# Kernel optimization log

Measured on AMD Instinct MI355X. Metric: run time of the kernel, lower is better.

The kernel has to match this reference:

```python
import jax, jax.numpy as jnp
import numpy as np

B, T, D = 8, 16384, 128


def setup_inputs() -> dict:
    key = jax.random.key(0)
    ks = jax.random.split(key, 14)
    sc = lambda fan_in: 1.0 / np.sqrt(fan_in)
    x = jax.random.normal(ks[0], (B, T, D), jnp.float32)
    return {
        "x": x,
        # BindingField (scale 0): bind_key / bind_query Linear(D, D//2)
        "Wk": jax.random.normal(ks[1], (D, D // 2), jnp.float32) * sc(D),
        "bk": jnp.zeros((D // 2,), jnp.float32),
        "Wq": jax.random.normal(ks[2], (D, D // 2), jnp.float32) * sc(D),
        "bq": jnp.zeros((D // 2,), jnp.float32),
        # aggregator (scale 0): Linear(D,D) -> LayerNorm(D) -> ReLU -> Linear(D,D)
        "Wa1": jax.random.normal(ks[3], (D, D), jnp.float32) * sc(D),
        "ba1": jnp.zeros((D,), jnp.float32),
        "ln_g": jnp.ones((D,), jnp.float32),
        "ln_b": jnp.zeros((D,), jnp.float32),
        "Wa2": jax.random.normal(ks[4], (D, D), jnp.float32) * sc(D),
        "ba2": jnp.zeros((D,), jnp.float32),
        # downward_influence (scale 0): Linear(D,D)
        "Wd": jax.random.normal(ks[5], (D, D), jnp.float32) * sc(D),
        "bd": jnp.zeros((D,), jnp.float32),
    }


def reference(x, Wk, bk, Wq, bq, Wa1, ba1, ln_g, ln_b, Wa2, ba2, Wd, bd):
    Bn, Tn, Dn = x.shape
    BIND_THRESHOLD = 0.5
    LN_EPS = 1e-5

    # ---- BindingField: binding strength between adjacent tokens ----
    keys = x[:, :-1] @ Wk + bk                       # [B, T-1, D/2]
    queries = x[:, 1:] @ Wq + bq                     # [B, T-1, D/2]
    strength = jax.nn.sigmoid((keys * queries).sum(-1) / float(np.sqrt(Dn // 2)))
    bind = strength > BIND_THRESHOLD                 # [B, T-1]

    # chunk_starts: token 0 always starts; token t starts iff NOT bound to t-1
    chunk_starts = jnp.concatenate([jnp.ones((Bn, 1), bool), ~bind], axis=1)
    seg = jnp.cumsum(chunk_starts.astype(jnp.int32), axis=1) - 1  # [B, T] chunk id per token

    # ---- aggregate_chunks: ragged mean-pool via segment_sum (pad to T chunk slots) ----
    seg_flat = (seg + jnp.arange(Bn, dtype=jnp.int32)[:, None] * Tn).reshape(-1)
    sums = jax.ops.segment_sum(x.reshape(-1, Dn), seg_flat, num_segments=Bn * Tn)
    counts = jax.ops.segment_sum(jnp.ones((Bn * Tn,), x.dtype), seg_flat,
                                 num_segments=Bn * Tn)
    chunk_mean = (sums / jnp.maximum(counts, 1.0)[:, None]).reshape(Bn, Tn, Dn)

    # aggregator MLP: Linear -> LayerNorm -> ReLU -> Linear
    h = chunk_mean @ Wa1 + ba1
    mu = h.mean(-1, keepdims=True)
    var = ((h - mu) ** 2).mean(-1, keepdims=True)    # biased var, as torch LayerNorm
    h = (h - mu) * jax.lax.rsqrt(var + LN_EPS) * ln_g + ln_b
    agg = jax.nn.relu(h) @ Wa2 + ba2                 # [B, T(chunk slots), D]

    # ---- apply_downward_influence: broadcast chunk signal back to its tokens ----
    infl = agg @ Wd + bd                             # [B, T(chunks), D]
    gathered = jnp.take_along_axis(infl, seg[..., None].astype(jnp.int32), axis=1)
    gate = jax.nn.sigmoid(gathered)
    return x * gate + x
```

## Files before the change

kernel.cpp:

```cpp
#include <hip/hip_runtime.h>
#include <math.h>

#define BB 8
#define TT 16384
#define DD 128
#define DH 64
#define FCAP 32768
#define FMARGIN 0.05f

typedef _Float16 half8 __attribute__((ext_vector_type(8)));
typedef float f32x4 __attribute__((ext_vector_type(4)));

union H8 { half8 h; uint4 q; ushort us[8]; };

static __device__ __forceinline__ float4 ld4(const float* p) { return *(const float4*)p; }

static __device__ __forceinline__ uint pk2(float a, float b) {
    union { _Float16 f; ushort u; } A, B;
    A.f = (_Float16)a; B.f = (_Float16)b;
    return (uint)A.u | ((uint)B.u << 16);
}

static __device__ __forceinline__ void split8h(const float4 v0, const float4 v1,
                                               half8* xh, half8* xl)
{
    float f[8] = {v0.x, v0.y, v0.z, v0.w, v1.x, v1.y, v1.z, v1.w};
    half8 h, l;
    #pragma unroll
    for (int j = 0; j < 8; ++j) {
        _Float16 hv = (_Float16)f[j];
        h[j] = hv;
        l[j] = (_Float16)(f[j] - (float)hv);
    }
    *xh = h; *xl = l;
}

__global__ __launch_bounds__(64) void k_wprep(
    const float* __restrict__ Wa1, const float* __restrict__ Wa2,
    const float* __restrict__ Wd, const float* __restrict__ Wk,
    const float* __restrict__ Wq, ushort* __restrict__ wfm,
    ushort* __restrict__ wfb, int* __restrict__ fcnt)
{
    const int l  = threadIdx.x;
    const int nt = blockIdx.x & 7;
    const int kb = blockIdx.x >> 3;
    const int ly = blockIdx.y;
    if (ly == 0 && blockIdx.x == 0 && l == 0) *fcnt = 0;
    const int n  = nt * 16 + (l & 15);
    const int k0 = kb * 32 + (l >> 4) * 8;
    H8 v;
    if (ly < 3) {
        const float* W = (ly == 0) ? Wa1 : (ly == 1) ? Wa2 : Wd;
        #pragma unroll
        for (int e = 0; e < 8; ++e) v.h[e] = (_Float16)W[(k0 + e) * DD + n];
        *(uint4*)(wfm + (size_t)(((ly * 8 + nt) * 4 + kb) * 64 + l) * 8) = v.q;
    } else {
        #pragma unroll
        for (int e = 0; e < 8; ++e) {
            float w = (n < 64) ? Wk[(k0 + e) * DH + n] : Wq[(k0 + e) * DH + n - 64];
            v.h[e] = (_Float16)w;
        }
        *(uint4*)(wfb + (size_t)((nt * 4 + kb) * 64 + l) * 8) = v.q;
    }
}

__global__ __launch_bounds__(256, 2) void k_bind(
    const float* __restrict__ x, const ushort* __restrict__ wfb,
    const float* __restrict__ bk, const float* __restrict__ bq,
    int* __restrict__ cstart, int* __restrict__ flist, int* __restrict__ fcnt)
{
    __shared__ uint4 Bs4[2048];
    __shared__ float bnd[4][64];
    const int b    = blockIdx.y;
    const int tb   = blockIdx.x * 64;
    const int tid  = threadIdx.x;
    const int wv   = tid >> 6;
    const int l    = tid & 63;
    const int lo16 = l & 15;
    const int g    = l >> 4;

    {
        const uint4* wsrc = (const uint4*)wfb;
        #pragma unroll
        for (int j = 0; j < 8; ++j) { int idx = tid + j * 256; Bs4[idx] = wsrc[idx]; }
    }

    const float* xrow = x + ((size_t)b * TT + tb + wv * 16 + lo16) * DD;
    half8 xh[4], xl[4];
    #pragma unroll
    for (int kb = 0; kb < 4; ++kb) {
        float4 v0 = ld4(xrow + kb * 32 + g * 8);
        float4 v1 = ld4(xrow + kb * 32 + g * 8 + 4);
        split8h(v0, v1, &xh[kb], &xl[kb]);
    }
    int r64 = tb + 64; if (r64 > TT - 1) r64 = TT - 1;
    const float* xq = x + ((size_t)b * TT + r64) * DD;
    half8 qh[4], ql[4];
    H8 z; z.q.x = z.q.y = z.q.z = z.q.w = 0u;
    #pragma unroll
    for (int kb = 0; kb < 4; ++kb) {
        qh[kb] = z.h; ql[kb] = z.h;
        if (lo16 == 0) {
            float4 v0 = ld4(xq + kb * 32 + g * 8);
            float4 v1 = ld4(xq + kb * 32 + g * 8 + 4);
            split8h(v0, v1, &qh[kb], &ql[kb]);
        }
    }

    f32x4 acc[8];
    #pragma unroll
    for (int nt = 0; nt < 8; ++nt) {
        int col = nt * 16 + lo16;
        float bias = (col < 64) ? bk[col] : bq[col - 64];
        acc[nt] = (f32x4){bias, bias, bias, bias};
    }
    f32x4 acc4;
    {
        float bias = bq[wv * 16 + lo16];
        acc4 = (f32x4){bias, bias, bias, bias};
    }

    __syncthreads();
    const ushort* Bs = (const ushort*)Bs4;
    const ushort* Bs_halo = Bs + (size_t)((4 + wv) * 4 * 64 + l) * 8;
    #pragma unroll
    for (int kb = 0; kb < 4; ++kb) {
        half8 bh[8];
        #pragma unroll
        for (int nt = 0; nt < 8; ++nt)
            bh[nt] = *(const half8*)(Bs + (size_t)((nt * 4 + kb) * 64 + l) * 8);
        #pragma unroll
        for (int nt = 0; nt < 8; ++nt) {
            acc[nt] = __builtin_amdgcn_mfma_f32_16x16x32_f16(xh[kb], bh[nt], acc[nt], 0, 0, 0);
            acc[nt] = __builtin_amdgcn_mfma_f32_16x16x32_f16(xl[kb], bh[nt], acc[nt], 0, 0, 0);
        }
        half8 bh4 = *(const half8*)(Bs_halo + (size_t)kb * 64 * 8);
        acc4 = __builtin_amdgcn_mfma_f32_16x16x32_f16(qh[kb], bh4, acc4, 0, 0, 0);
        acc4 = __builtin_amdgcn_mfma_f32_16x16x32_f16(ql[kb], bh4, acc4, 0, 0, 0);
    }

    if (l < 16) {
        if (wv > 0) {
            #pragma unroll
            for (int nt = 0; nt < 4; ++nt) bnd[wv - 1][nt * 16 + lo16] = acc[4 + nt][0];
        }
        bnd[3][wv * 16 + lo16] = acc4[0];
    }
    __syncthreads();

    float qn3[4];
    #pragma unroll
    for (int nt = 0; nt < 4; ++nt) qn3[nt] = __shfl_down(acc[4 + nt][0], 16);
    if (g == 3) {
        #pragma unroll
        for (int nt = 0; nt < 4; ++nt) qn3[nt] = bnd[wv][nt * 16 + lo16];
    }
    float s[4];
    #pragma unroll
    for (int i = 0; i < 3; ++i) {
        float t = 0.f;
        #pragma unroll
        for (int nt = 0; nt < 4; ++nt) t += acc[nt][i] * acc[4 + nt][i + 1];
        s[i] = t;
    }
    {
        float t = 0.f;
        #pragma unroll
        for (int nt = 0; nt < 4; ++nt) t += acc[nt][3] * qn3[nt];
        s[3] = t;
    }
    #pragma unroll
    for (int i = 0; i < 4; ++i) {
        #pragma unroll
        for (int m = 1; m < 16; m <<= 1) s[i] += __shfl_xor(s[i], m);
    }
    if (lo16 == 0) {
        #pragma unroll
        for (int i = 0; i < 4; ++i) {
            int t = tb + wv * 16 + g * 4 + i;
            if (t <= TT - 2) {
                cstart[b * TT + t + 1] = (s[i] > 0.f) ? 0 : 1;
                if (fabsf(s[i]) < FMARGIN) {
                    int pos = atomicAdd(fcnt, 1);
                    if (pos < FCAP) flist[pos] = b * TT + t;
                }
            }
        }
    }
    if (blockIdx.x == 0 && tid == 0) cstart[b * TT] = 1;
}

__global__ __launch_bounds__(256) void k_fixup(
    const float* __restrict__ x, const float* __restrict__ Wk, const float* __restrict__ bk,
    const float* __restrict__ Wq, const float* __restrict__ bq,
    const int* __restrict__ flist, const int* __restrict__ fcnt, int* __restrict__ cstart)
{
    const int n    = min(*fcnt, FCAP);
    const int wv   = (blockIdx.x * 256 + threadIdx.x) >> 6;
    const int lane = threadIdx.x & 63;
    const int nwv  = gridDim.x * 4;
    for (int i = wv; i < n; i += nwv) {
        int idx = flist[i];
        int b = idx >> 14;
        int t = idx & (TT - 1);
        const float* xt = x + ((size_t)b * TT + t) * DD;
        float K = bk[lane], Q = bq[lane];
        #pragma unroll 8
        for (int k = 0; k < DD; ++k) {
            K = fmaf(xt[k],      Wk[k * DH + lane], K);
            Q = fmaf(xt[DD + k], Wq[k * DH + lane], Q);
        }
        float p = K * Q;
        #pragma unroll
        for (int m = 1; m < 64; m <<= 1) p += __shfl_xor(p, m);
        if (lane == 0) cstart[b * TT + t + 1] = (p > 0.f) ? 0 : 1;
    }
}

__global__ __launch_bounds__(1024) void k_scan(const int* __restrict__ cstart,
    int* __restrict__ seg, int* __restrict__ cs, int* __restrict__ numC)
{
    __shared__ int wsum[16];
    const int b = blockIdx.x, tid = threadIdx.x;
    const int wv = tid >> 6, lane = tid & 63;
    const int base = b * TT + tid * 16;
    int v[16];
    #pragma unroll
    for (int i = 0; i < 4; ++i) {
        int4 q = *(const int4*)(cstart + base + i * 4);
        v[i * 4 + 0] = q.x; v[i * 4 + 1] = q.y; v[i * 4 + 2] = q.z; v[i * 4 + 3] = q.w;
    }
    int s[16]; int run = 0;
    #pragma unroll
    for (int i = 0; i < 16; ++i) { run += v[i]; s[i] = run; }
    int incl = run;
    #pragma unroll
    for (int off = 1; off < 64; off <<= 1) {
        int t = __shfl_up(incl, off);
        if (lane >= off) incl += t;
    }
    if (lane == 63) wsum[wv] = incl;
    __syncthreads();
    if (tid < 16) {
        int w = wsum[tid];
        #pragma unroll
        for (int off = 1; off < 16; off <<= 1) {
            int t = __shfl_up(w, off, 16);
            if (tid >= off) w += t;
        }
        wsum[tid] = w;
    }
    __syncthreads();
    const int excl = (wv ? wsum[wv - 1] : 0) + incl - run;
    #pragma unroll
    for (int i = 0; i < 16; ++i) {
        int sg = excl + s[i] - 1;
        seg[base + i] = sg;
        if (v[i]) cs[b * (TT + 1) + sg] = tid * 16 + i;
    }
    if (tid == 1023) {
        int tot = excl + run;
        numC[b] = tot;
        cs[b * (TT + 1) + tot] = TT;
    }
}

__device__ __forceinline__ void mlp_gemm(f32x4 acc[8], const uint4* Afr4,
    const ushort* Bs, int wv, int l)
{
    half8 af[4];
    #pragma unroll
    for (int kb = 0; kb < 4; ++kb)
        af[kb] = *(const half8*)((const char*)Afr4 + ((wv * 4 + kb) * 64 + l) * 16);
    #pragma unroll
    for (int kb = 0; kb < 4; ++kb) {
        half8 bh[8];
        #pragma unroll
        for (int nt = 0; nt < 8; ++nt)
            bh[nt] = *(const half8*)(Bs + (size_t)((nt * 4 + kb) * 64 + l) * 8);
        #pragma unroll
        for (int nt = 0; nt < 8; ++nt)
            acc[nt] = __builtin_amdgcn_mfma_f32_16x16x32_f16(af[kb], bh[nt], acc[nt], 0, 0, 0);
    }
}

__global__ __launch_bounds__(256, 2) void k_mlp(
    const float* __restrict__ x, const int* __restrict__ cs,
    const float* __restrict__ ba1, const float* __restrict__ ln_g, const float* __restrict__ ln_b,
    const float* __restrict__ ba2, const float* __restrict__ bd,
    const ushort* __restrict__ wfm, const int* __restrict__ numC, float* __restrict__ cm)
{
    __shared__ union {
        float Tok[2][32 * 128];
        struct { uint4 Afr[1024]; uint4 Bs[2048]; } fb;
    } sm;
    const int b  = blockIdx.y;
    const int nC = numC[b];
    const int c0 = blockIdx.x * 64;
    if (c0 >= nC) return;
    const int tid  = threadIdx.x;
    const int wv   = tid >> 6;
    const int l    = tid & 63;
    const int lo16 = l & 15;
    const int g    = l >> 4;
    const ushort* Bs = (const ushort*)sm.fb.Bs;
    const uint4* wsrc = (const uint4*)wfm;

    const int cbase = b * (TT + 1);
    const int T0 = cs[cbase + c0];
    const int cEnd = (c0 + 64 < nC) ? (c0 + 64) : nC;
    const int T1 = cs[cbase + cEnd];
    int t0r[8], t1r[8];
    #pragma unroll
    for (int ii = 0; ii < 8; ++ii) {
        int r = (tid + ii * 256) >> 5;
        int c = c0 + r;
        t0r[ii] = (c < nC) ? cs[cbase + c] : 0;
        t1r[ii] = (c < nC) ? cs[cbase + c + 1] : 0;
    }
    float4 vals[8];
    #pragma unroll
    for (int ii = 0; ii < 8; ++ii) vals[ii] = make_float4(0.f, 0.f, 0.f, 0.f);

    {
        const int n16 = ((T0 + 32 < T1) ? 32 : (T1 - T0)) * 32;
        #pragma unroll
        for (int j = 0; j < 4; ++j) {
            int base16 = j * 256 + wv * 64;
            if (base16 + l < n16) {
                const float* gs = x + ((size_t)b * TT + T0) * DD + (size_t)(base16 + l) * 4;
                __builtin_amdgcn_global_load_lds(
                    (const __attribute__((address_space(1))) void*)gs,
                    (__attribute__((address_space(3))) void*)&sm.Tok[0][base16 * 4],
                    16, 0, 0);
            }
        }
    }
    int buf = 0;
    for (int tt = T0; tt < T1; tt += 32) {
        asm volatile("s_waitcnt vmcnt(0)" ::: "memory");
        __syncthreads();
        const int tEnd = (tt + 32 < T1) ? (tt + 32) : T1;
        if (tt + 32 < T1) {
            const int nEnd = (tt + 64 < T1) ? (tt + 64) : T1;
            const int n16 = (nEnd - (tt + 32)) * 32;
            #pragma unroll
            for (int j = 0; j < 4; ++j) {
                int base16 = j * 256 + wv * 64;
                if (base16 + l < n16) {
                    const float* gs = x + ((size_t)b * TT + tt + 32) * DD + (size_t)(base16 + l) * 4;
                    __builtin_amdgcn_global_load_lds(
                        (const __attribute__((address_space(1))) void*)gs,
                        (__attribute__((address_space(3))) void*)&sm.Tok[buf ^ 1][base16 * 4],
                        16, 0, 0);
                }
            }
        }
        #pragma unroll
        for (int ii = 0; ii < 8; ++ii) {
            int c4 = ((tid + ii * 256) & 31) * 4;
            int lo = (t0r[ii] > tt)   ? t0r[ii] : tt;
            int hi = (t1r[ii] < tEnd) ? t1r[ii] : tEnd;
            for (int t = lo; t < hi; ++t) {
                const float* ap = &sm.Tok[buf][(t - tt) * 128 + c4];
                vals[ii].x += ap[0]; vals[ii].y += ap[1];
                vals[ii].z += ap[2]; vals[ii].w += ap[3];
            }
        }
        buf ^= 1;
    }
    asm volatile("s_waitcnt vmcnt(0)" ::: "memory");
    __syncthreads();

    #pragma unroll
    for (int ii = 0; ii < 8; ++ii) {
        int i = tid + ii * 256;
        int r = i >> 5, c4 = (i & 31) * 4;
        float4 sv = make_float4(0.f, 0.f, 0.f, 0.f);
        if (c0 + r < nC) {
            float inv = 1.f / (float)(t1r[ii] - t0r[ii]);
            sv.x = vals[ii].x * inv; sv.y = vals[ii].y * inv;
            sv.z = vals[ii].z * inv; sv.w = vals[ii].w * inv;
        }
        int frag = (r >> 4) * 4 + (c4 >> 5);
        int lanef = (r & 15) + (((c4 & 31) >> 3) * 16);
        uint2 pk = make_uint2(pk2(sv.x, sv.y), pk2(sv.z, sv.w));
        *(uint2*)((char*)sm.fb.Afr + frag * 1024 + lanef * 16 + (c4 & 7) * 2) = pk;
    }
    #pragma unroll
    for (int j = 0; j < 8; ++j) { int idx = tid + j * 256; sm.fb.Bs[idx] = wsrc[idx]; }
    __syncthreads();

    f32x4 acc[8];
    #pragma unroll
    for (int nt = 0; nt < 8; ++nt) {
        float bias = ba1[nt * 16 + lo16];
        acc[nt] = (f32x4){bias, bias, bias, bias};
    }
    mlp_gemm(acc, sm.fb.Afr, Bs, wv, l);

    float mu_[4], rs_[4];
    #pragma unroll
    for (int i = 0; i < 4; ++i) {
        float smv = 0.f;
        #pragma unroll
        for (int nt = 0; nt < 8; ++nt) smv += acc[nt][i];
        #pragma unroll
        for (int k = 1; k < 16; k <<= 1) smv += __shfl_xor(smv, k, 16);
        mu_[i] = smv * (1.f / 128.f);
        float vs = 0.f;
        #pragma unroll
        for (int nt = 0; nt < 8; ++nt) { float d = acc[nt][i] - mu_[i]; vs += d * d; }
        #pragma unroll
        for (int k = 1; k < 16; k <<= 1) vs += __shfl_xor(vs, k, 16);
        rs_[i] = rsqrtf(vs * (1.f / 128.f) + 1e-5f);
    }
    float gam[8], bet[8];
    #pragma unroll
    for (int nt = 0; nt < 8; ++nt) { gam[nt] = ln_g[nt * 16 + lo16]; bet[nt] = ln_b[nt * 16 + lo16]; }

    __syncthreads();
    #pragma unroll
    for (int nt = 0; nt < 8; ++nt) {
        int cw = nt * 16 + lo16;
        int frag = wv * 4 + (cw >> 5);
        int lnf  = (((cw & 31) >> 3) * 16);
        #pragma unroll
        for (int i = 0; i < 4; ++i) {
            float h = fmaf((acc[nt][i] - mu_[i]) * rs_[i], gam[nt], bet[nt]);
            union { _Float16 f; ushort u; } cv; cv.f = (_Float16)fmaxf(h, 0.f);
            *((ushort*)((char*)sm.fb.Afr + frag * 1024 + ((g * 4 + i) + lnf) * 16 + (cw & 7) * 2)) = cv.u;
        }
    }
    #pragma unroll
    for (int j = 0; j < 8; ++j) { int idx = tid + j * 256; sm.fb.Bs[idx] = wsrc[2048 + idx]; }
    __syncthreads();

    #pragma unroll
    for (int nt = 0; nt < 8; ++nt) {
        float bias = ba2[nt * 16 + lo16];
        acc[nt] = (f32x4){bias, bias, bias, bias};
    }
    mlp_gemm(acc, sm.fb.Afr, Bs, wv, l);
    __syncthreads();
    #pragma unroll
    for (int nt = 0; nt < 8; ++nt) {
        int cw = nt * 16 + lo16;
        int frag = wv * 4 + (cw >> 5);
        int lnf  = (((cw & 31) >> 3) * 16);
        #pragma unroll
        for (int i = 0; i < 4; ++i) {
            union { _Float16 f; ushort u; } cv; cv.f = (_Float16)acc[nt][i];
            *((ushort*)((char*)sm.fb.Afr + frag * 1024 + ((g * 4 + i) + lnf) * 16 + (cw & 7) * 2)) = cv.u;
        }
    }
    #pragma unroll
    for (int j = 0; j < 8; ++j) { int idx = tid + j * 256; sm.fb.Bs[idx] = wsrc[4096 + idx]; }
    __syncthreads();

    #pragma unroll
    for (int nt = 0; nt < 8; ++nt) {
        float bias = bd[nt * 16 + lo16];
        acc[nt] = (f32x4){bias, bias, bias, bias};
    }
    mlp_gemm(acc, sm.fb.Afr, Bs, wv, l);
    #pragma unroll
    for (int i = 0; i < 4; ++i) {
        int row = c0 + wv * 16 + g * 4 + i;
        if (row < nC) {
            float* dst = cm + ((size_t)b * TT + row) * DD + lo16;
            #pragma unroll
            for (int nt = 0; nt < 8; ++nt)
                dst[nt * 16] = 1.f / (1.f + __expf(-acc[nt][i]));
        }
    }
}

__global__ __launch_bounds__(256) void k_out(const float* __restrict__ x,
    const int* __restrict__ seg, const float* __restrict__ gate, float* __restrict__ out)
{
    const size_t idx = (size_t)blockIdx.x * 256 + threadIdx.x;
    const size_t tok = idx >> 5;
    const int d4 = (int)(idx & 31);
    const int b  = (int)(tok >> 14);
    const int sg = seg[tok];
    float4 gv = ld4(gate + (((size_t)b << 14) + sg) * DD + d4 * 4);
    float4 xv = ld4(x + tok * DD + (size_t)d4 * 4);
    float4 o;
    o.x = fmaf(xv.x, gv.x, xv.x);
    o.y = fmaf(xv.y, gv.y, xv.y);
    o.z = fmaf(xv.z, gv.z, xv.z);
    o.w = fmaf(xv.w, gv.w, xv.w);
    *(float4*)(out + idx * 4) = o;
}

extern "C" void kernel_launch(void* const* d_in, const int* in_sizes, int n_in,
                              void* d_out, int out_size, void* d_ws, size_t ws_size,
                              hipStream_t stream)
{
    (void)in_sizes; (void)n_in; (void)out_size; (void)ws_size;
    const float* x    = (const float*)d_in[0];
    const float* Wk   = (const float*)d_in[1];
    const float* bk   = (const float*)d_in[2];
    const float* Wq   = (const float*)d_in[3];
    const float* bq   = (const float*)d_in[4];
    const float* Wa1  = (const float*)d_in[5];
    const float* ba1  = (const float*)d_in[6];
    const float* ln_g = (const float*)d_in[7];
    const float* ln_b = (const float*)d_in[8];
    const float* Wa2  = (const float*)d_in[9];
    const float* ba2  = (const float*)d_in[10];
    const float* Wd   = (const float*)d_in[11];
    const float* bd   = (const float*)d_in[12];
    float* out = (float*)d_out;

    char* p = (char*)d_ws;
    float* cm    = (float*)p;   p += (size_t)BB * TT * DD * 4;
    int* seg     = (int*)p;     p += (size_t)BB * TT * 4;
    int* cs      = (int*)p;     p += (size_t)BB * (TT + 1) * 4;
    int* numC    = (int*)p;     p += 64;
    ushort* wfm  = (ushort*)p;  p += 3 * DD * DD * 2;
    ushort* wfb  = (ushort*)p;  p += DD * DD * 2;
    int* flist   = (int*)p;     p += (size_t)FCAP * 4;
    int* fcnt    = (int*)p;

    k_wprep<<<dim3(32, 4), 64, 0, stream>>>(Wa1, Wa2, Wd, Wk, Wq, wfm, wfb, fcnt);
    k_bind<<<dim3(256, BB), 256, 0, stream>>>(x, wfb, bk, bq, seg, flist, fcnt);
    k_fixup<<<dim3(256), 256, 0, stream>>>(x, Wk, bk, Wq, bq, flist, fcnt, seg);
    k_scan<<<dim3(BB), 1024, 0, stream>>>(seg, seg, cs, numC);
    k_mlp<<<dim3(TT / 64, BB), 256, 0, stream>>>(x, cs, ba1, ln_g, ln_b, ba2, bd, wfm, numC, cm);
    k_out<<<dim3(BB * TT * DD / (256 * 4)), 256, 0, stream>>>(x, seg, cm, out);
}
```

Baseline: 113.9 us.

## Interleave ragged chunk sums and async-load MLP weights into LDS

The per-thread chunk accumulation loop now steps all eight owned chunks together up to the longest length, instead of running each chunk's variable-length loop in sequence. This exposes independent LDS reads and adds across chunks but executes predicated-off iterations for shorter chunks. The three MLP weight-tile copies to LDS now use global_load_lds issued before the fragment-packing work, with a vmcnt wait before the barrier. This is meant to hide weight-load latency behind the packing and drop the register round trip.

```diff
diff --git a/kernel.cpp b/kernel.cpp
--- a/kernel.cpp
+++ b/kernel.cpp
@@ -356,22 +356,41 @@
                 }
             }
         }
-        #pragma unroll
-        for (int ii = 0; ii < 8; ++ii) {
-            int c4 = ((tid + ii * 256) & 31) * 4;
-            int lo = (t0r[ii] > tt)   ? t0r[ii] : tt;
-            int hi = (t1r[ii] < tEnd) ? t1r[ii] : tEnd;
-            for (int t = lo; t < hi; ++t) {
-                const float* ap = &sm.Tok[buf][(t - tt) * 128 + c4];
-                vals[ii].x += ap[0]; vals[ii].y += ap[1];
-                vals[ii].z += ap[2]; vals[ii].w += ap[3];
+        {
+            int lo_[8], hi_[8];
+            int ml = 0;
+            #pragma unroll
+            for (int ii = 0; ii < 8; ++ii) {
+                lo_[ii] = (t0r[ii] > tt)   ? t0r[ii] : tt;
+                hi_[ii] = (t1r[ii] < tEnd) ? t1r[ii] : tEnd;
+                int len = hi_[ii] - lo_[ii];
+                if (len > ml) ml = len;
             }
+            for (int st = 0; st < ml; ++st) {
+                #pragma unroll
+                for (int ii = 0; ii < 8; ++ii) {
+                    int t = lo_[ii] + st;
+                    if (t < hi_[ii]) {
+                        int c4 = ((tid + ii * 256) & 31) * 4;
+                        const float* ap = &sm.Tok[buf][(t - tt) * 128 + c4];
+                        vals[ii].x += ap[0]; vals[ii].y += ap[1];
+                        vals[ii].z += ap[2]; vals[ii].w += ap[3];
+                    }
+                }
+            }
         }
         buf ^= 1;
     }
     asm volatile("s_waitcnt vmcnt(0)" ::: "memory");
     __syncthreads();
 
+    #pragma unroll
+    for (int j = 0; j < 8; ++j) {
+        int idx = tid + j * 256;
+        __builtin_amdgcn_global_load_lds(
+            (const __attribute__((address_space(1))) void*)(wsrc + idx),
+            (__attribute__((address_space(3))) void*)&sm.fb.Bs[idx], 16, 0, 0);
+    }
     #pragma unroll
     for (int ii = 0; ii < 8; ++ii) {
         int i = tid + ii * 256;
@@ -387,8 +406,7 @@
         uint2 pk = make_uint2(pk2(sv.x, sv.y), pk2(sv.z, sv.w));
         *(uint2*)((char*)sm.fb.Afr + frag * 1024 + lanef * 16 + (c4 & 7) * 2) = pk;
     }
-    #pragma unroll
-    for (int j = 0; j < 8; ++j) { int idx = tid + j * 256; sm.fb.Bs[idx] = wsrc[idx]; }
+    asm volatile("s_waitcnt vmcnt(0)" ::: "memory");
     __syncthreads();
 
     f32x4 acc[8];
@@ -420,6 +438,13 @@
     for (int nt = 0; nt < 8; ++nt) { gam[nt] = ln_g[nt * 16 + lo16]; bet[nt] = ln_b[nt * 16 + lo16]; }
 
     __syncthreads();
+    #pragma unroll
+    for (int j = 0; j < 8; ++j) {
+        int idx = tid + j * 256;
+        __builtin_amdgcn_global_load_lds(
+            (const __attribute__((address_space(1))) void*)(wsrc + 2048 + idx),
+            (__attribute__((address_space(3))) void*)&sm.fb.Bs[idx], 16, 0, 0);
+    }
     #pragma unroll
     for (int nt = 0; nt < 8; ++nt) {
         int cw = nt * 16 + lo16;
@@ -432,8 +457,7 @@
             *((ushort*)((char*)sm.fb.Afr + frag * 1024 + ((g * 4 + i) + lnf) * 16 + (cw & 7) * 2)) = cv.u;
         }
     }
-    #pragma unroll
-    for (int j = 0; j < 8; ++j) { int idx = tid + j * 256; sm.fb.Bs[idx] = wsrc[2048 + idx]; }
+    asm volatile("s_waitcnt vmcnt(0)" ::: "memory");
     __syncthreads();
 
     #pragma unroll
@@ -443,6 +467,13 @@
     }
     mlp_gemm(acc, sm.fb.Afr, Bs, wv, l);
     __syncthreads();
+    #pragma unroll
+    for (int j = 0; j < 8; ++j) {
+        int idx = tid + j * 256;
+        __builtin_amdgcn_global_load_lds(
+            (const __attribute__((address_space(1))) void*)(wsrc + 4096 + idx),
+            (__attribute__((address_space(3))) void*)&sm.fb.Bs[idx], 16, 0, 0);
+    }
     #pragma unroll
     for (int nt = 0; nt < 8; ++nt) {
         int cw = nt * 16 + lo16;
@@ -454,8 +485,7 @@
             *((ushort*)((char*)sm.fb.Afr + frag * 1024 + ((g * 4 + i) + lnf) * 16 + (cw & 7) * 2)) = cv.u;
         }
     }
-    #pragma unroll
-    for (int j = 0; j < 8; ++j) { int idx = tid + j * 256; sm.fb.Bs[idx] = wsrc[4096 + idx]; }
+    asm volatile("s_waitcnt vmcnt(0)" ::: "memory");
     __syncthreads();
 
     #pragma unroll
```

Result: slower. 122.7 us (+7.7%).
